# Optimization experiments

Measured on AMD Instinct MI355X. Metric: run time of the kernel, lower is better.

## Reference

```python
import jax, jax.numpy as jnp
import numpy as np

B, S, E = 4, 2048, 1024
H, HD, R = 16, 64, 32  # heads, head_dim, rank


def setup_inputs() -> dict:
    key = jax.random.key(0)
    ks = jax.random.split(key, 9)
    sc = 0.02
    return {
        "hidden_states": jax.random.normal(ks[0], (B, S, E), jnp.float32),
        "q_weight": jax.random.normal(ks[1], (E, E), jnp.float32) * sc,
        "q_bias": jax.random.normal(ks[2], (E,), jnp.float32) * sc,
        "k_weight": jax.random.normal(ks[3], (E, E), jnp.float32) * sc,
        "k_bias": jax.random.normal(ks[4], (E,), jnp.float32) * sc,
        "low_rank_value_weight": jax.random.normal(ks[5], (E, H * R), jnp.float32) * sc,
        "low_rank_value_bias": jax.random.normal(ks[6], (H * R,), jnp.float32) * sc,
        "low_rank_output_weight": jax.random.normal(ks[7], (H * R, E), jnp.float32) * sc,
        "output_bias": jax.random.normal(ks[8], (E,), jnp.float32) * sc,
    }


def reference(hidden_states, q_weight, q_bias, k_weight, k_bias,
              low_rank_value_weight, low_rank_value_bias,
              low_rank_output_weight, output_bias):
    b, s, _ = hidden_states.shape
    q = hidden_states @ q_weight + q_bias                       # [B,S,E]
    k = hidden_states @ k_weight + k_bias                       # [B,S,E]
    v = hidden_states @ low_rank_value_weight + low_rank_value_bias  # [B,S,H*R]
    q = q.reshape(b, s, H, HD).transpose(0, 2, 1, 3)            # [B,H,S,HD]
    k = k.reshape(b, s, H, HD).transpose(0, 2, 1, 3)
    v = v.reshape(b, s, H, R).transpose(0, 2, 1, 3)             # [B,H,S,R]
    scores = jnp.einsum('bhqd,bhkd->bhqk', q, k) / jnp.sqrt(jnp.float32(HD))
    causal = jnp.tril(jnp.ones((s, s), dtype=bool))
    scores = jnp.where(causal, scores, jnp.finfo(scores.dtype).min)
    probs = jax.nn.softmax(scores, axis=-1)                     # [B,H,S,S]
    attn = jnp.einsum('bhqk,bhkr->bhqr', probs, v)              # [B,H,S,R]
    attn = attn.transpose(0, 2, 1, 3).reshape(b, s, H * R)      # [B,S,H*R]
    out = attn @ low_rank_output_weight + output_bias           # [B,S,E]
    return out
```

## Files before the change

kernel.cpp:

```cpp
#include <hip/hip_runtime.h>

typedef _Float16 f16;
typedef __attribute__((ext_vector_type(4))) float f4;
typedef __attribute__((ext_vector_type(4))) _Float16 h4;
typedef __attribute__((ext_vector_type(8))) _Float16 h8;
typedef __attribute__((ext_vector_type(4))) float f32x4;
typedef __attribute__((ext_vector_type(4))) unsigned int u4;

extern "C" __device__ __attribute__((const)) float __ocml_native_exp2_f32(float);
#define EXP2F __ocml_native_exp2_f32
#define L2E 1.4426950408889634f

#define SWZ(row, colByte) \
  (((row) << 7) + ((colByte) ^ (((((row) ^ ((row) >> 3))) & 7) << 4)))

#define GL16(gp, lp)                                                  \
  __builtin_amdgcn_global_load_lds(                                   \
      (const __attribute__((address_space(1))) unsigned int*)(gp),    \
      (__attribute__((address_space(3))) unsigned int*)(lp), 16, 0, 0)

__global__ __launch_bounds__(256) void prep(
    const float* __restrict__ hs, f16* __restrict__ hsf,
    const float* __restrict__ qw, const float* __restrict__ kw,
    const float* __restrict__ vw, const float* __restrict__ ow,
    f16* __restrict__ wqkv, f16* __restrict__ owt) {
  const int t = threadIdx.x;
  if (blockIdx.x < 2048) {
    const int n4 = 8192 * 1024 / 4;
    for (int i = blockIdx.x * 256 + t; i < n4; i += 2048 * 256) {
      const f4 v = ((const f4*)hs)[i];
      h4 h;
      h.x = (f16)v.x; h.y = (f16)v.y; h.z = (f16)v.z; h.w = (f16)v.w;
      ((h4*)hsf)[i] = h;
    }
    return;
  }
  __shared__ float tile[32][33];
  int bid = blockIdx.x - 2048;
  const float* in;
  f16* out;
  int R, C, bx, by;
  if (bid < 1024) {
    in = qw; out = wqkv; R = 1024; C = 1024; bx = bid & 31; by = bid >> 5;
  } else if (bid < 2048) {
    bid -= 1024;
    in = kw; out = wqkv + (size_t)1024 * 1024; R = 1024; C = 1024;
    bx = bid & 31; by = bid >> 5;
  } else if (bid < 2560) {
    bid -= 2048;
    in = vw; out = wqkv + (size_t)2048 * 1024; R = 1024; C = 512;
    bx = bid & 15; by = bid >> 4;
  } else {
    bid -= 2560;
    in = ow; out = owt; R = 512; C = 1024; bx = bid & 31; by = bid >> 5;
  }
  const int tx = t & 31, ty = t >> 5;
  const int bc = bx * 32, br = by * 32;
#pragma unroll
  for (int i = 0; i < 4; ++i)
    tile[ty + i * 8][tx] = in[(size_t)(br + ty + i * 8) * C + bc + tx];
  __syncthreads();
#pragma unroll
  for (int i = 0; i < 4; ++i)
    out[(size_t)(bc + ty + i * 8) * R + br + tx] = (f16)tile[tx][ty + i * 8];
}

__global__ __launch_bounds__(256) void hgemm_qkv(
    const f16* __restrict__ A, const f16* __restrict__ Bt,
    const float* __restrict__ qb, const float* __restrict__ kb,
    const float* __restrict__ vb,
    f16* __restrict__ qf, f16* __restrict__ kf, f16* __restrict__ vf) {
  __shared__ f16 As[2 * 128 * 32];
  __shared__ f16 Bs[2 * 128 * 32];
  const int K = 1024;
  const int id = blockIdx.x;
  const int xcd = id & 7, loc = id >> 3;
  const int grp = loc >> 5, inn = loc & 31;
  const int bnT = grp * 4 + (inn >> 3);
  const int bm = (xcd * 8 + (inn & 7)) * 128;
  const int bn = bnT * 128;
  const int t = threadIdx.x;
  const int lane = t & 63, wave = t >> 6;
  const int wr = wave >> 1, wc = wave & 1;
  const int lrow = lane & 15, lk = lane >> 4;
  const int srow = lane >> 2;
  const int sblk = (lane & 3) ^ ((srow ^ (srow >> 2)) & 3);

  f32x4 acc[4][4];
#pragma unroll
  for (int i = 0; i < 4; ++i)
#pragma unroll
    for (int j = 0; j < 4; ++j) acc[i][j] = (f32x4)0.f;

  auto stage = [&](int buf, int ktile) {
#pragma unroll
    for (int i = 0; i < 2; ++i) {
      const int rr = (wave * 2 + i) * 16 + srow;
      GL16(A + (size_t)(bm + rr) * K + ktile * 32 + sblk * 8,
           (char*)As + buf * 8192 + (wave * 2 + i) * 1024);
      GL16(Bt + (size_t)(bn + rr) * K + ktile * 32 + sblk * 8,
           (char*)Bs + buf * 8192 + (wave * 2 + i) * 1024);
    }
  };

  stage(0, 0);
  for (int kt = 0; kt < 32; ++kt) {
    const int cur = kt & 1;
    stage(cur ^ 1, (kt + 1) & 31);
    asm volatile("s_waitcnt vmcnt(4)" ::: "memory");
    __builtin_amdgcn_s_barrier();
    __builtin_amdgcn_sched_barrier(0);
    h8 af[4], bf[4];
#pragma unroll
    for (int f = 0; f < 4; ++f) {
      const int ra = wr * 64 + f * 16 + lrow;
      af[f] = *(const h8*)((char*)As + cur * 8192 + ra * 64 +
                           ((lk ^ ((ra ^ (ra >> 2)) & 3)) << 4));
      const int rb = wc * 64 + f * 16 + lrow;
      bf[f] = *(const h8*)((char*)Bs + cur * 8192 + rb * 64 +
                           ((lk ^ ((rb ^ (rb >> 2)) & 3)) << 4));
    }
#pragma unroll
    for (int i2 = 0; i2 < 4; ++i2)
#pragma unroll
      for (int j = 0; j < 4; ++j)
        acc[i2][j] = __builtin_amdgcn_mfma_f32_16x16x32_f16(af[i2], bf[j], acc[i2][j], 0, 0, 0);
    asm volatile("s_waitcnt lgkmcnt(0)" ::: "memory");
    __builtin_amdgcn_sched_barrier(0);
    __builtin_amdgcn_s_barrier();
  }

  const float* bias;
  int nbase;
  if (bnT < 8) { bias = qb; nbase = 0; }
  else if (bnT < 16) { bias = kb; nbase = 1024; }
  else { bias = vb; nbase = 2048; }

#pragma unroll
  for (int fi = 0; fi < 4; ++fi) {
#pragma unroll
    for (int j = 0; j < 4; ++j) {
      const int grow = bm + wr * 64 + fi * 16 + lk * 4 + j;
      const int bb = grow >> 11, ss = grow & 2047;
#pragma unroll
      for (int fj = 0; fj < 4; ++fj) {
        const int gcol = bn + wc * 64 + fj * 16 + lrow;
        const int nl = gcol - nbase;
        const float g = acc[fi][fj][j] + bias[nl];
        if (bnT < 8) {
          qf[((size_t)(bb * 16 + (nl >> 6)) * 2048 + ss) * 64 + (nl & 63)] = (f16)g;
        } else if (bnT < 16) {
          kf[((size_t)(bb * 16 + (nl >> 6)) * 2048 + ss) * 64 + (nl & 63)] = (f16)g;
        } else {
          vf[((size_t)(bb * 16 + (nl >> 5)) * 2048 + ss) * 32 + (nl & 31)] = (f16)g;
        }
      }
    }
  }
}

__global__ __launch_bounds__(256) void transpose_v(
    const f16* __restrict__ vf, f16* __restrict__ vfT) {
  __shared__ f16 tl[32][36];
  const int bh = blockIdx.x >> 6;
  const int st = (blockIdx.x & 63) * 32;
  const int t = threadIdx.x;
  const int row = t >> 3, cq = t & 7;
  {
    const h4 v = *(const h4*)(vf + ((size_t)bh * 2048 + st + row) * 32 + cq * 4);
    *(h4*)&tl[row][cq * 4] = v;
  }
  __syncthreads();
  {
    h4 v;
#pragma unroll
    for (int e = 0; e < 4; ++e) v[e] = tl[cq * 4 + e][row];
    *(h4*)(vfT + ((size_t)bh * 32 + row) * 2048 + st + cq * 4) = v;
  }
}

__global__ __launch_bounds__(256) void hgemm_out(
    const f16* __restrict__ A, const f16* __restrict__ Bt,
    const float* __restrict__ bias, float* __restrict__ outp,
    const int N, const int K) {
  __shared__ f16 As[128 * 40];
  __shared__ f16 Bs[128 * 40];
  const int id = blockIdx.x;
  const int swz = (id & 7) * 64 + (id >> 3);
  const int bn = (swz & 7) * 128;
  const int bm = (swz >> 3) * 128;
  const int t = threadIdx.x;
  const int lane = t & 63, wave = t >> 6;
  const int wr = wave >> 1, wc = wave & 1;
  const int lrow = lane & 15, lk = lane >> 4;

  f32x4 acc[4][4];
#pragma unroll
  for (int i = 0; i < 4; ++i)
#pragma unroll
    for (int j = 0; j < 4; ++j) acc[i][j] = (f32x4)0.f;

  for (int kt = 0; kt < K; kt += 32) {
#pragma unroll
    for (int i = 0; i < 2; ++i) {
      const int ch = t + i * 256;
      const int row = ch >> 2, part = ch & 3;
      *(u4*)&As[row * 40 + part * 8] =
          *(const u4*)(A + (size_t)(bm + row) * K + kt + part * 8);
      *(u4*)&Bs[row * 40 + part * 8] =
          *(const u4*)(Bt + (size_t)(bn + row) * K + kt + part * 8);
    }
    __syncthreads();
    h8 af[4], bf[4];
#pragma unroll
    for (int f = 0; f < 4; ++f) {
      af[f] = *(const h8*)&As[(wr * 64 + f * 16 + lrow) * 40 + lk * 8];
      bf[f] = *(const h8*)&Bs[(wc * 64 + f * 16 + lrow) * 40 + lk * 8];
    }
#pragma unroll
    for (int i = 0; i < 4; ++i)
#pragma unroll
      for (int j = 0; j < 4; ++j)
        acc[i][j] = __builtin_amdgcn_mfma_f32_16x16x32_f16(af[i], bf[j], acc[i][j], 0, 0, 0);
    __syncthreads();
  }

#pragma unroll
  for (int fi = 0; fi < 4; ++fi) {
#pragma unroll
    for (int j = 0; j < 4; ++j) {
      const int grow = bm + wr * 64 + fi * 16 + lk * 4 + j;
#pragma unroll
      for (int fj = 0; fj < 4; ++fj) {
        const int gcol = bn + wc * 64 + fj * 16 + lrow;
        outp[(size_t)grow * N + gcol] = acc[fi][fj][j] + bias[gcol];
      }
    }
  }
}

__global__ __launch_bounds__(256) void attn_mfma(
    const f16* __restrict__ qf, const f16* __restrict__ kf,
    const f16* __restrict__ vfT, f16* __restrict__ attf) {
  __shared__ f16 Ks[2][64 * 64];
  __shared__ f16 VsT[2][32 * 64];
  __shared__ f16 Ps[4 * 32 * 64];
  const int id = blockIdx.x;
  const int bh = id & 63;
  const int p = id >> 6;
  const int t = threadIdx.x;
  const int lane = t & 63, w = t >> 6;
  const int l15 = lane & 15, g = lane >> 4;
  const size_t kvbase = (size_t)bh * 2048;
  char* Pw = (char*)&Ps[w * 32 * 64];
  const int srow = t >> 3, sch = t & 7;
  const int b = bh >> 4, h = bh & 15;

  h8 ones;
#pragma unroll
  for (int e = 0; e < 8; ++e) ones[e] = (f16)1.0f;

#pragma unroll
  for (int run = 0; run < 2; ++run) {
    const int qblk = run ? p : 15 - p;
    const int qbase = qblk * 128;

    h8 qreg[2][2];
#pragma unroll
    for (int fj = 0; fj < 2; ++fj) {
      const int q = qbase + fj * 64 + w * 16 + l15;
#pragma unroll
      for (int ks = 0; ks < 2; ++ks) {
        h8 raw = *(const h8*)(qf + (kvbase + q) * 64 + ks * 32 + g * 8);
#pragma unroll
        for (int e = 0; e < 8; ++e) raw[e] = raw[e] * (f16)0.125f;
        qreg[fj][ks] = raw;
      }
    }

    f32x4 accO[2][2];
    f32x4 accL[2];
#pragma unroll
    for (int i = 0; i < 2; ++i) {
      accL[i] = (f32x4)0.f;
#pragma unroll
      for (int j = 0; j < 2; ++j) accO[i][j] = (f32x4)0.f;
    }
    float m2[2] = {-1.0e30f, -1.0e30f};

    const int ntiles = qblk * 2 + 2;

    {
      const u4 k0 = *(const u4*)(kf + (kvbase + srow) * 64 + sch * 8);
      const u4 k1 = *(const u4*)(kf + (kvbase + 32 + srow) * 64 + sch * 8);
      const u4 v0 = *(const u4*)(vfT + ((size_t)bh * 32 + srow) * 2048 + sch * 8);
      *(u4*)((char*)&Ks[0][0] + SWZ(srow, sch * 16)) = k0;
      *(u4*)((char*)&Ks[0][0] + SWZ(srow + 32, sch * 16)) = k1;
      *(u4*)((char*)&VsT[0][0] + SWZ(srow, sch * 16)) = v0;
    }
    __syncthreads();

    u4 kr0, kr1, vr0;
    for (int kt = 0; kt < ntiles; ++kt) {
      const int cur = kt & 1;
      const int kbase = kt * 64;
      const bool more = (kt + 1 < ntiles);
      if (more) {
        const int kb2 = kbase + 64;
        kr0 = *(const u4*)(kf + (kvbase + kb2 + srow) * 64 + sch * 8);
        kr1 = *(const u4*)(kf + (kvbase + kb2 + 32 + srow) * 64 + sch * 8);
        vr0 = *(const u4*)(vfT + ((size_t)bh * 32 + srow) * 2048 + kb2 + sch * 8);
      }

      f32x4 accS[4][2];
#pragma unroll
      for (int i = 0; i < 4; ++i)
#pragma unroll
        for (int j = 0; j < 2; ++j) accS[i][j] = (f32x4)0.f;
#pragma unroll
      for (int ks = 0; ks < 2; ++ks) {
#pragma unroll
        for (int fim = 0; fim < 4; ++fim) {
          const h8 af = *(const h8*)((char*)&Ks[cur][0] +
                                     SWZ(fim * 16 + l15, ks * 64 + g * 16));
#pragma unroll
          for (int fj = 0; fj < 2; ++fj)
            accS[fim][fj] = __builtin_amdgcn_mfma_f32_16x16x32_f16(
                af, qreg[fj][ks], accS[fim][fj], 0, 0, 0);
        }
      }

#pragma unroll
      for (int fj = 0; fj < 2; ++fj) {
        const int qg = qbase + fj * 64 + w * 16 + l15;
        const bool need_mask = (kbase + 63 > qbase + fj * 64 + w * 16);
        float sc[4][4];
#pragma unroll
        for (int fim = 0; fim < 4; ++fim)
#pragma unroll
          for (int j = 0; j < 4; ++j) {
            float v = accS[fim][fj][j];
            if (need_mask) {
              const int key = kbase + fim * 16 + g * 4 + j;
              v = (key <= qg) ? v : -1.0e30f;
            }
            sc[fim][j] = v;
          }
        const float a0 = fmaxf(fmaxf(sc[0][0], sc[0][1]), sc[0][2]);
        const float a1 = fmaxf(fmaxf(sc[0][3], sc[1][0]), sc[1][1]);
        const float a2 = fmaxf(fmaxf(sc[1][2], sc[1][3]), sc[2][0]);
        const float a3 = fmaxf(fmaxf(sc[2][1], sc[2][2]), sc[2][3]);
        const float a4 = fmaxf(fmaxf(sc[3][0], sc[3][1]), sc[3][2]);
        float mc = fmaxf(fmaxf(fmaxf(a0, a1), a2),
                         fmaxf(fmaxf(a3, a4), sc[3][3]));
        mc = fmaxf(mc, __shfl_xor(mc, 16));
        mc = fmaxf(mc, __shfl_xor(mc, 32));
        if (!__all(mc <= m2[fj] + 1.5f)) {
          const float mnew = fmaxf(m2[fj], mc);
          const float corr = __expf(m2[fj] - mnew);
          m2[fj] = mnew;
#pragma unroll
          for (int j = 0; j < 4; ++j) {
            const float c = __shfl(corr, g * 4 + j);
            accO[fj][0][j] *= c;
            accO[fj][1][j] *= c;
            accL[fj][j] *= c;
          }
        }
        const float nml = -m2[fj] * L2E;
#pragma unroll
        for (int fim = 0; fim < 4; ++fim) {
          h4 hp;
#pragma unroll
          for (int j = 0; j < 4; ++j)
            hp[j] = (f16)EXP2F(fmaf(sc[fim][j], L2E, nml));
          *(h4*)(Pw + SWZ(fj * 16 + l15, fim * 32 + g * 8)) = hp;
        }
      }

#pragma unroll
      for (int ks = 0; ks < 2; ++ks) {
        const h8 pa0 = *(const h8*)(Pw + SWZ(l15, ks * 64 + g * 16));
        const h8 pa1 = *(const h8*)(Pw + SWZ(16 + l15, ks * 64 + g * 16));
#pragma unroll
        for (int fr = 0; fr < 2; ++fr) {
          const h8 vb = *(const h8*)((char*)&VsT[cur][0] +
                                     SWZ(fr * 16 + l15, ks * 64 + g * 16));
          accO[0][fr] = __builtin_amdgcn_mfma_f32_16x16x32_f16(pa0, vb, accO[0][fr], 0, 0, 0);
          accO[1][fr] = __builtin_amdgcn_mfma_f32_16x16x32_f16(pa1, vb, accO[1][fr], 0, 0, 0);
        }
        accL[0] = __builtin_amdgcn_mfma_f32_16x16x32_f16(pa0, ones, accL[0], 0, 0, 0);
        accL[1] = __builtin_amdgcn_mfma_f32_16x16x32_f16(pa1, ones, accL[1], 0, 0, 0);
      }

      if (more) {
        *(u4*)((char*)&Ks[cur ^ 1][0] + SWZ(srow, sch * 16)) = kr0;
        *(u4*)((char*)&Ks[cur ^ 1][0] + SWZ(srow + 32, sch * 16)) = kr1;
        *(u4*)((char*)&VsT[cur ^ 1][0] + SWZ(srow, sch * 16)) = vr0;
      }
      __syncthreads();
    }

#pragma unroll
    for (int fo = 0; fo < 2; ++fo) {
#pragma unroll
      for (int j = 0; j < 4; ++j) {
        const float iv = 1.f / accL[fo][j];
        const int q = qbase + fo * 64 + w * 16 + g * 4 + j;
#pragma unroll
        for (int fr = 0; fr < 2; ++fr) {
          const int r = fr * 16 + l15;
          attf[((size_t)b * 2048 + q) * 512 + h * 32 + r] = (f16)(accO[fo][fr][j] * iv);
        }
      }
    }
    __syncthreads();
  }
}

extern "C" void kernel_launch(void* const* d_in, const int* in_sizes, int n_in,
                              void* d_out, int out_size, void* d_ws, size_t ws_size,
                              hipStream_t stream) {
  const float* hs = (const float*)d_in[0];
  const float* qw = (const float*)d_in[1];
  const float* qb = (const float*)d_in[2];
  const float* kw = (const float*)d_in[3];
  const float* kb = (const float*)d_in[4];
  const float* vw = (const float*)d_in[5];
  const float* vb = (const float*)d_in[6];
  const float* ow = (const float*)d_in[7];
  const float* ob = (const float*)d_in[8];
  float* out = (float*)d_out;
  char* ws = (char*)d_ws;

  f16* qf = (f16*)(ws);
  f16* kf = (f16*)(ws + ((size_t)16 << 20));
  f16* vf = (f16*)(ws + ((size_t)32 << 20));
  f16* vfT = (f16*)(ws + ((size_t)72 << 20));
  f16* attf = (f16*)(ws + ((size_t)40 << 20));
  f16* wqkv = (f16*)(ws + ((size_t)48 << 20));
  f16* owt = (f16*)(ws + ((size_t)53 << 20));
  f16* hsf = (f16*)(ws + ((size_t)56 << 20));

  prep<<<dim3(5120), 256, 0, stream>>>(hs, hsf, qw, kw, vw, ow, wqkv, owt);
  hgemm_qkv<<<dim3(1280), 256, 0, stream>>>(hsf, wqkv, qb, kb, vb, qf, kf, vf);
  transpose_v<<<dim3(4096), 256, 0, stream>>>(vf, vfT);
  attn_mfma<<<dim3(512), 256, 0, stream>>>(qf, kf, vfT, attf);
  hgemm_out<<<dim3(512), 256, 0, stream>>>(attf, owt, ob, out, 1024, 512);
}
```

Before: 162.9 us.

## Widen attention blocks to 512 threads with 256-query tiles and per-wave causal skip

The attention kernel now uses 8 waves per block, and each block covers 256 queries instead of 128, so every K/V tile loaded into shared memory is reused by twice as many queries. The grid is halved to 256 blocks. Each wave tracks the last key tile its own query rows need and skips MFMA and softmax work on tiles past its causal limit, so waves early in the block idle while later waves finish. The risks are fewer blocks than compute units, worse load balance from the larger causal pairing granularity, and more register pressure under the 512-thread launch bound.

After: 173.1 us. 1.06x slower.

```diff
diff --git a/kernel.cpp b/kernel.cpp
--- a/kernel.cpp
+++ b/kernel.cpp
@@ -239,12 +239,12 @@
   }
 }
 
-__global__ __launch_bounds__(256) void attn_mfma(
+__global__ __launch_bounds__(512) void attn_mfma(
     const f16* __restrict__ qf, const f16* __restrict__ kf,
     const f16* __restrict__ vfT, f16* __restrict__ attf) {
   __shared__ f16 Ks[2][64 * 64];
   __shared__ f16 VsT[2][32 * 64];
-  __shared__ f16 Ps[4 * 32 * 64];
+  __shared__ f16 Ps[8 * 32 * 64];
   const int id = blockIdx.x;
   const int bh = id & 63;
   const int p = id >> 6;
@@ -252,7 +252,7 @@
   const int lane = t & 63, w = t >> 6;
   const int l15 = lane & 15, g = lane >> 4;
   const size_t kvbase = (size_t)bh * 2048;
-  char* Pw = (char*)&Ps[w * 32 * 64];
+  char* Pw = (char*)Ps + w * 4096;
   const int srow = t >> 3, sch = t & 7;
   const int b = bh >> 4, h = bh & 15;
 
@@ -260,15 +260,17 @@
 #pragma unroll
   for (int e = 0; e < 8; ++e) ones[e] = (f16)1.0f;
 
-#pragma unroll
   for (int run = 0; run < 2; ++run) {
-    const int qblk = run ? p : 15 - p;
-    const int qbase = qblk * 128;
+    const int qblk = run ? p : 7 - p;
+    const int qbase = qblk * 256;
+    const int ntiles = qblk * 4 + 4;
+    const int wl0 = (qbase + w * 16 + 15) >> 6;
+    const int wl1 = (qbase + 128 + w * 16 + 15) >> 6;
 
     h8 qreg[2][2];
 #pragma unroll
     for (int fj = 0; fj < 2; ++fj) {
-      const int q = qbase + fj * 64 + w * 16 + l15;
+      const int q = qbase + fj * 128 + w * 16 + l15;
 #pragma unroll
       for (int ks = 0; ks < 2; ++ks) {
         h8 raw = *(const h8*)(qf + (kvbase + q) * 64 + ks * 32 + g * 8);
@@ -288,115 +290,124 @@
     }
     float m2[2] = {-1.0e30f, -1.0e30f};
 
-    const int ntiles = qblk * 2 + 2;
-
     {
       const u4 k0 = *(const u4*)(kf + (kvbase + srow) * 64 + sch * 8);
-      const u4 k1 = *(const u4*)(kf + (kvbase + 32 + srow) * 64 + sch * 8);
-      const u4 v0 = *(const u4*)(vfT + ((size_t)bh * 32 + srow) * 2048 + sch * 8);
       *(u4*)((char*)&Ks[0][0] + SWZ(srow, sch * 16)) = k0;
-      *(u4*)((char*)&Ks[0][0] + SWZ(srow + 32, sch * 16)) = k1;
-      *(u4*)((char*)&VsT[0][0] + SWZ(srow, sch * 16)) = v0;
+      if (t < 256) {
+        const u4 v0 = *(const u4*)(vfT + ((size_t)bh * 32 + (t >> 3)) * 2048 + sch * 8);
+        *(u4*)((char*)&VsT[0][0] + SWZ(t >> 3, sch * 16)) = v0;
+      }
     }
     __syncthreads();
 
-    u4 kr0, kr1, vr0;
+    u4 kr, vr;
     for (int kt = 0; kt < ntiles; ++kt) {
       const int cur = kt & 1;
       const int kbase = kt * 64;
       const bool more = (kt + 1 < ntiles);
       if (more) {
         const int kb2 = kbase + 64;
-        kr0 = *(const u4*)(kf + (kvbase + kb2 + srow) * 64 + sch * 8);
-        kr1 = *(const u4*)(kf + (kvbase + kb2 + 32 + srow) * 64 + sch * 8);
-        vr0 = *(const u4*)(vfT + ((size_t)bh * 32 + srow) * 2048 + kb2 + sch * 8);
-      }
-
-      f32x4 accS[4][2];
-#pragma unroll
-      for (int i = 0; i < 4; ++i)
-#pragma unroll
-        for (int j = 0; j < 2; ++j) accS[i][j] = (f32x4)0.f;
-#pragma unroll
-      for (int ks = 0; ks < 2; ++ks) {
-#pragma unroll
-        for (int fim = 0; fim < 4; ++fim) {
-          const h8 af = *(const h8*)((char*)&Ks[cur][0] +
-                                     SWZ(fim * 16 + l15, ks * 64 + g * 16));
-#pragma unroll
-          for (int fj = 0; fj < 2; ++fj)
-            accS[fim][fj] = __builtin_amdgcn_mfma_f32_16x16x32_f16(
-                af, qreg[fj][ks], accS[fim][fj], 0, 0, 0);
-        }
-      }
-
-#pragma unroll
-      for (int fj = 0; fj < 2; ++fj) {
-        const int qg = qbase + fj * 64 + w * 16 + l15;
-        const bool need_mask = (kbase + 63 > qbase + fj * 64 + w * 16);
-        float sc[4][4];
-#pragma unroll
-        for (int fim = 0; fim < 4; ++fim)
-#pragma unroll
-          for (int j = 0; j < 4; ++j) {
-            float v = accS[fim][fj][j];
-            if (need_mask) {
-              const int key = kbase + fim * 16 + g * 4 + j;
-              v = (key <= qg) ? v : -1.0e30f;
-            }
-            sc[fim][j] = v;
-          }
-        const float a0 = fmaxf(fmaxf(sc[0][0], sc[0][1]), sc[0][2]);
-        const float a1 = fmaxf(fmaxf(sc[0][3], sc[1][0]), sc[1][1]);
-        const float a2 = fmaxf(fmaxf(sc[1][2], sc[1][3]), sc[2][0]);
-        const float a3 = fmaxf(fmaxf(sc[2][1], sc[2][2]), sc[2][3]);
-        const float a4 = fmaxf(fmaxf(sc[3][0], sc[3][1]), sc[3][2]);
-        float mc = fmaxf(fmaxf(fmaxf(a0, a1), a2),
-                         fmaxf(fmaxf(a3, a4), sc[3][3]));
-        mc = fmaxf(mc, __shfl_xor(mc, 16));
-        mc = fmaxf(mc, __shfl_xor(mc, 32));
-        if (!__all(mc <= m2[fj] + 1.5f)) {
-          const float mnew = fmaxf(m2[fj], mc);
-          const float corr = __expf(m2[fj] - mnew);
-          m2[fj] = mnew;
-#pragma unroll
-          for (int j = 0; j < 4; ++j) {
-            const float c = __shfl(corr, g * 4 + j);
-            accO[fj][0][j] *= c;
-            accO[fj][1][j] *= c;
-            accL[fj][j] *= c;
+        kr = *(const u4*)(kf + (kvbase + kb2 + srow) * 64 + sch * 8);
+        if (t < 256)
+          vr = *(const u4*)(vfT + ((size_t)bh * 32 + (t >> 3)) * 2048 + kb2 + sch * 8);
+      }
+
+      if (kt <= wl1) {
+        const bool do0 = (kt <= wl0);
+
+        f32x4 accS[4][2];
+#pragma unroll
+        for (int i = 0; i < 4; ++i)
+#pragma unroll
+          for (int j = 0; j < 2; ++j) accS[i][j] = (f32x4)0.f;
+#pragma unroll
+        for (int ks = 0; ks < 2; ++ks) {
+#pragma unroll
+          for (int fim = 0; fim < 4; ++fim) {
+            const h8 af = *(const h8*)((char*)&Ks[cur][0] +
+                                       SWZ(fim * 16 + l15, ks * 64 + g * 16));
+            if (do0)
+              accS[fim][0] = __builtin_amdgcn_mfma_f32_16x16x32_f16(
+                  af, qreg[0][ks], accS[fim][0], 0, 0, 0);
+            accS[fim][1] = __builtin_amdgcn_mfma_f32_16x16x32_f16(
+                af, qreg[1][ks], accS[fim][1], 0, 0, 0);
           }
         }
-        const float nml = -m2[fj] * L2E;
-#pragma unroll
-        for (int fim = 0; fim < 4; ++fim) {
-          h4 hp;
-#pragma unroll
-          for (int j = 0; j < 4; ++j)
-            hp[j] = (f16)EXP2F(fmaf(sc[fim][j], L2E, nml));
-          *(h4*)(Pw + SWZ(fj * 16 + l15, fim * 32 + g * 8)) = hp;
+
+#pragma unroll
+        for (int fj = 0; fj < 2; ++fj) {
+          if (fj == 0 && !do0) continue;
+          const int qg = qbase + fj * 128 + w * 16 + l15;
+          const bool need_mask = (kbase + 63 > qbase + fj * 128 + w * 16);
+          float sc[4][4];
+#pragma unroll
+          for (int fim = 0; fim < 4; ++fim)
+#pragma unroll
+            for (int j = 0; j < 4; ++j) {
+              float v = accS[fim][fj][j];
+              if (need_mask) {
+                const int key = kbase + fim * 16 + g * 4 + j;
+                v = (key <= qg) ? v : -1.0e30f;
+              }
+              sc[fim][j] = v;
+            }
+          const float a0 = fmaxf(fmaxf(sc[0][0], sc[0][1]), sc[0][2]);
+          const float a1 = fmaxf(fmaxf(sc[0][3], sc[1][0]), sc[1][1]);
+          const float a2 = fmaxf(fmaxf(sc[1][2], sc[1][3]), sc[2][0]);
+          const float a3 = fmaxf(fmaxf(sc[2][1], sc[2][2]), sc[2][3]);
+          const float a4 = fmaxf(fmaxf(sc[3][0], sc[3][1]), sc[3][2]);
+          float mc = fmaxf(fmaxf(fmaxf(a0, a1), a2),
+                           fmaxf(fmaxf(a3, a4), sc[3][3]));
+          mc = fmaxf(mc, __shfl_xor(mc, 16));
+          mc = fmaxf(mc, __shfl_xor(mc, 32));
+          if (!__all(mc <= m2[fj] + 1.5f)) {
+            const float mnew = fmaxf(m2[fj], mc);
+            const float corr = __expf(m2[fj] - mnew);
+            m2[fj] = mnew;
+#pragma unroll
+            for (int j = 0; j < 4; ++j) {
+              const float c = __shfl(corr, g * 4 + j);
+              accO[fj][0][j] *= c;
+              accO[fj][1][j] *= c;
+              accL[fj][j] *= c;
+            }
+          }
+          const float nml = -m2[fj] * L2E;
+#pragma unroll
+          for (int fim = 0; fim < 4; ++fim) {
+            h4 hp;
+#pragma unroll
+            for (int j = 0; j < 4; ++j)
+              hp[j] = (f16)EXP2F(fmaf(sc[fim][j], L2E, nml));
+            *(h4*)(Pw + SWZ(fj * 16 + l15, fim * 32 + g * 8)) = hp;
+          }
         }
-      }
-
-#pragma unroll
-      for (int ks = 0; ks < 2; ++ks) {
-        const h8 pa0 = *(const h8*)(Pw + SWZ(l15, ks * 64 + g * 16));
-        const h8 pa1 = *(const h8*)(Pw + SWZ(16 + l15, ks * 64 + g * 16));
-#pragma unroll
-        for (int fr = 0; fr < 2; ++fr) {
-          const h8 vb = *(const h8*)((char*)&VsT[cur][0] +
-                                     SWZ(fr * 16 + l15, ks * 64 + g * 16));
-          accO[0][fr] = __builtin_amdgcn_mfma_f32_16x16x32_f16(pa0, vb, accO[0][fr], 0, 0, 0);
-          accO[1][fr] = __builtin_amdgcn_mfma_f32_16x16x32_f16(pa1, vb, accO[1][fr], 0, 0, 0);
+
+#pragma unroll
+        for (int ks = 0; ks < 2; ++ks) {
+          const h8 pa1 = *(const h8*)(Pw + SWZ(16 + l15, ks * 64 + g * 16));
+#pragma unroll
+          for (int fr = 0; fr < 2; ++fr) {
+            const h8 vb = *(const h8*)((char*)&VsT[cur][0] +
+                                       SWZ(fr * 16 + l15, ks * 64 + g * 16));
+            if (do0) {
+              const h8 pa0 = *(const h8*)(Pw + SWZ(l15, ks * 64 + g * 16));
+              accO[0][fr] = __builtin_amdgcn_mfma_f32_16x16x32_f16(pa0, vb, accO[0][fr], 0, 0, 0);
+            }
+            accO[1][fr] = __builtin_amdgcn_mfma_f32_16x16x32_f16(pa1, vb, accO[1][fr], 0, 0, 0);
+          }
+          if (do0) {
+            const h8 pa0 = *(const h8*)(Pw + SWZ(l15, ks * 64 + g * 16));
+            accL[0] = __builtin_amdgcn_mfma_f32_16x16x32_f16(pa0, ones, accL[0], 0, 0, 0);
+          }
+          accL[1] = __builtin_amdgcn_mfma_f32_16x16x32_f16(pa1, ones, accL[1], 0, 0, 0);
         }
-        accL[0] = __builtin_amdgcn_mfma_f32_16x16x32_f16(pa0, ones, accL[0], 0, 0, 0);
-        accL[1] = __builtin_amdgcn_mfma_f32_16x16x32_f16(pa1, ones, accL[1], 0, 0, 0);
       }
 
       if (more) {
-        *(u4*)((char*)&Ks[cur ^ 1][0] + SWZ(srow, sch * 16)) = kr0;
-        *(u4*)((char*)&Ks[cur ^ 1][0] + SWZ(srow + 32, sch * 16)) = kr1;
-        *(u4*)((char*)&VsT[cur ^ 1][0] + SWZ(srow, sch * 16)) = vr0;
+        *(u4*)((char*)&Ks[cur ^ 1][0] + SWZ(srow, sch * 16)) = kr;
+        if (t < 256)
+          *(u4*)((char*)&VsT[cur ^ 1][0] + SWZ(t >> 3, sch * 16)) = vr;
       }
       __syncthreads();
     }
@@ -406,7 +417,7 @@
 #pragma unroll
       for (int j = 0; j < 4; ++j) {
         const float iv = 1.f / accL[fo][j];
-        const int q = qbase + fo * 64 + w * 16 + g * 4 + j;
+        const int q = qbase + fo * 128 + w * 16 + g * 4 + j;
 #pragma unroll
         for (int fr = 0; fr < 2; ++fr) {
           const int r = fr * 16 + l15;
@@ -445,6 +456,6 @@
   prep<<<dim3(5120), 256, 0, stream>>>(hs, hsf, qw, kw, vw, ow, wqkv, owt);
   hgemm_qkv<<<dim3(1280), 256, 0, stream>>>(hsf, wqkv, qb, kb, vb, qf, kf, vf);
   transpose_v<<<dim3(4096), 256, 0, stream>>>(vf, vfT);
-  attn_mfma<<<dim3(512), 256, 0, stream>>>(qf, kf, vfT, attf);
+  attn_mfma<<<dim3(256), 512, 0, stream>>>(qf, kf, vfT, attf);
   hgemm_out<<<dim3(512), 256, 0, stream>>>(attf, owt, ob, out, 1024, 512);
 }
```

## Halve attention query tile to 64 rows and double grid size

Applied to the files above, without the earlier changes.

The attention kernel now processes 64 queries per block (16 per wave) instead of 128. The grid doubles to 1024 blocks, each still pairing a short and a long causal block for balance. This raises parallelism and occupancy through fewer registers and a smaller P buffer in shared memory. In exchange, each K/V tile loaded into shared memory is reused by half as many queries. The change also adds s_setprio around the MFMA sections and stops unrolling the run loop.

Result: slower. 177.1 us (+8.7%).

```diff
diff --git a/kernel.cpp b/kernel.cpp
--- a/kernel.cpp
+++ b/kernel.cpp
@@ -244,7 +244,7 @@
     const f16* __restrict__ vfT, f16* __restrict__ attf) {
   __shared__ f16 Ks[2][64 * 64];
   __shared__ f16 VsT[2][32 * 64];
-  __shared__ f16 Ps[4 * 32 * 64];
+  __shared__ f16 Ps[4 * 16 * 64];
   const int id = blockIdx.x;
   const int bh = id & 63;
   const int p = id >> 6;
@@ -252,7 +252,7 @@
   const int lane = t & 63, w = t >> 6;
   const int l15 = lane & 15, g = lane >> 4;
   const size_t kvbase = (size_t)bh * 2048;
-  char* Pw = (char*)&Ps[w * 32 * 64];
+  char* Pw = (char*)Ps + w * 2048;
   const int srow = t >> 3, sch = t & 7;
   const int b = bh >> 4, h = bh & 15;
 
@@ -260,35 +260,27 @@
 #pragma unroll
   for (int e = 0; e < 8; ++e) ones[e] = (f16)1.0f;
 
-#pragma unroll
   for (int run = 0; run < 2; ++run) {
-    const int qblk = run ? p : 15 - p;
-    const int qbase = qblk * 128;
-
-    h8 qreg[2][2];
-#pragma unroll
-    for (int fj = 0; fj < 2; ++fj) {
-      const int q = qbase + fj * 64 + w * 16 + l15;
-#pragma unroll
-      for (int ks = 0; ks < 2; ++ks) {
-        h8 raw = *(const h8*)(qf + (kvbase + q) * 64 + ks * 32 + g * 8);
-#pragma unroll
-        for (int e = 0; e < 8; ++e) raw[e] = raw[e] * (f16)0.125f;
-        qreg[fj][ks] = raw;
-      }
-    }
-
-    f32x4 accO[2][2];
-    f32x4 accL[2];
-#pragma unroll
-    for (int i = 0; i < 2; ++i) {
-      accL[i] = (f32x4)0.f;
-#pragma unroll
-      for (int j = 0; j < 2; ++j) accO[i][j] = (f32x4)0.f;
-    }
-    float m2[2] = {-1.0e30f, -1.0e30f};
-
-    const int ntiles = qblk * 2 + 2;
+    const int qblk = run ? p : 31 - p;
+    const int qbase = qblk * 64;
+    const int ntiles = qblk + 1;
+    const int qg = qbase + w * 16 + l15;
+
+    h8 qreg[2];
+#pragma unroll
+    for (int ks = 0; ks < 2; ++ks) {
+      h8 raw = *(const h8*)(qf + (kvbase + qg) * 64 + ks * 32 + g * 8);
+#pragma unroll
+      for (int e = 0; e < 8; ++e) raw[e] = raw[e] * (f16)0.125f;
+      qreg[ks] = raw;
+    }
+
+    f32x4 accO[2];
+    f32x4 accL;
+    accL = (f32x4)0.f;
+#pragma unroll
+    for (int j = 0; j < 2; ++j) accO[j] = (f32x4)0.f;
+    float m2 = -1.0e30f;
 
     {
       const u4 k0 = *(const u4*)(kf + (kvbase + srow) * 64 + sch * 8);
@@ -300,7 +292,7 @@
     }
     __syncthreads();
 
-    u4 kr0, kr1, vr0;
+    u4 kr0, kr1, vr;
     for (int kt = 0; kt < ntiles; ++kt) {
       const int cur = kt & 1;
       const int kbase = kt * 64;
@@ -309,37 +301,33 @@
         const int kb2 = kbase + 64;
         kr0 = *(const u4*)(kf + (kvbase + kb2 + srow) * 64 + sch * 8);
         kr1 = *(const u4*)(kf + (kvbase + kb2 + 32 + srow) * 64 + sch * 8);
-        vr0 = *(const u4*)(vfT + ((size_t)bh * 32 + srow) * 2048 + kb2 + sch * 8);
-      }
-
-      f32x4 accS[4][2];
-#pragma unroll
-      for (int i = 0; i < 4; ++i)
-#pragma unroll
-        for (int j = 0; j < 2; ++j) accS[i][j] = (f32x4)0.f;
+        vr = *(const u4*)(vfT + ((size_t)bh * 32 + srow) * 2048 + kb2 + sch * 8);
+      }
+
+      f32x4 accS[4];
+#pragma unroll
+      for (int i = 0; i < 4; ++i) accS[i] = (f32x4)0.f;
+      __builtin_amdgcn_s_setprio(1);
 #pragma unroll
       for (int ks = 0; ks < 2; ++ks) {
 #pragma unroll
         for (int fim = 0; fim < 4; ++fim) {
           const h8 af = *(const h8*)((char*)&Ks[cur][0] +
                                      SWZ(fim * 16 + l15, ks * 64 + g * 16));
-#pragma unroll
-          for (int fj = 0; fj < 2; ++fj)
-            accS[fim][fj] = __builtin_amdgcn_mfma_f32_16x16x32_f16(
-                af, qreg[fj][ks], accS[fim][fj], 0, 0, 0);
+          accS[fim] = __builtin_amdgcn_mfma_f32_16x16x32_f16(
+              af, qreg[ks], accS[fim], 0, 0, 0);
         }
       }
-
-#pragma unroll
-      for (int fj = 0; fj < 2; ++fj) {
-        const int qg = qbase + fj * 64 + w * 16 + l15;
-        const bool need_mask = (kbase + 63 > qbase + fj * 64 + w * 16);
+      __builtin_amdgcn_s_setprio(0);
+
+      {
+        const bool need_mask = (kbase + 63 > qbase + w * 16);
         float sc[4][4];
 #pragma unroll
         for (int fim = 0; fim < 4; ++fim)
 #pragma unroll
           for (int j = 0; j < 4; ++j) {
-            float v = accS[fim][fj][j];
+            float v = accS[fim][j];
             if (need_mask) {
               const int key = kbase + fim * 16 + g * 4 + j;
               v = (key <= qg) ? v : -1.0e30f;
@@ -355,63 +343,59 @@
                          fmaxf(fmaxf(a3, a4), sc[3][3]));
         mc = fmaxf(mc, __shfl_xor(mc, 16));
         mc = fmaxf(mc, __shfl_xor(mc, 32));
-        if (!__all(mc <= m2[fj] + 1.5f)) {
-          const float mnew = fmaxf(m2[fj], mc);
-          const float corr = __expf(m2[fj] - mnew);
-          m2[fj] = mnew;
+        if (!__all(mc <= m2 + 1.5f)) {
+          const float mnew = fmaxf(m2, mc);
+          const float corr = __expf(m2 - mnew);
+          m2 = mnew;
 #pragma unroll
           for (int j = 0; j < 4; ++j) {
             const float c = __shfl(corr, g * 4 + j);
-            accO[fj][0][j] *= c;
-            accO[fj][1][j] *= c;
-            accL[fj][j] *= c;
+            accO[0][j] *= c;
+            accO[1][j] *= c;
+            accL[j] *= c;
           }
         }
-        const float nml = -m2[fj] * L2E;
+        const float nml = -m2 * L2E;
 #pragma unroll
         for (int fim = 0; fim < 4; ++fim) {
           h4 hp;
 #pragma unroll
           for (int j = 0; j < 4; ++j)
             hp[j] = (f16)EXP2F(fmaf(sc[fim][j], L2E, nml));
-          *(h4*)(Pw + SWZ(fj * 16 + l15, fim * 32 + g * 8)) = hp;
+          *(h4*)(Pw + SWZ(l15, fim * 32 + g * 8)) = hp;
         }
       }
 
+      __builtin_amdgcn_s_setprio(1);
 #pragma unroll
       for (int ks = 0; ks < 2; ++ks) {
-        const h8 pa0 = *(const h8*)(Pw + SWZ(l15, ks * 64 + g * 16));
-        const h8 pa1 = *(const h8*)(Pw + SWZ(16 + l15, ks * 64 + g * 16));
+        const h8 pa = *(const h8*)(Pw + SWZ(l15, ks * 64 + g * 16));
 #pragma unroll
         for (int fr = 0; fr < 2; ++fr) {
           const h8 vb = *(const h8*)((char*)&VsT[cur][0] +
                                      SWZ(fr * 16 + l15, ks * 64 + g * 16));
-          accO[0][fr] = __builtin_amdgcn_mfma_f32_16x16x32_f16(pa0, vb, accO[0][fr], 0, 0, 0);
-          accO[1][fr] = __builtin_amdgcn_mfma_f32_16x16x32_f16(pa1, vb, accO[1][fr], 0, 0, 0);
+          accO[fr] = __builtin_amdgcn_mfma_f32_16x16x32_f16(pa, vb, accO[fr], 0, 0, 0);
         }
-        accL[0] = __builtin_amdgcn_mfma_f32_16x16x32_f16(pa0, ones, accL[0], 0, 0, 0);
-        accL[1] = __builtin_amdgcn_mfma_f32_16x16x32_f16(pa1, ones, accL[1], 0, 0, 0);
-      }
+        accL = __builtin_amdgcn_mfma_f32_16x16x32_f16(pa, ones, accL, 0, 0, 0);
+      }
+      __builtin_amdgcn_s_setprio(0);
 
       if (more) {
         *(u4*)((char*)&Ks[cur ^ 1][0] + SWZ(srow, sch * 16)) = kr0;
         *(u4*)((char*)&Ks[cur ^ 1][0] + SWZ(srow + 32, sch * 16)) = kr1;
-        *(u4*)((char*)&VsT[cur ^ 1][0] + SWZ(srow, sch * 16)) = vr0;
+        *(u4*)((char*)&VsT[cur ^ 1][0] + SWZ(srow, sch * 16)) = vr;
       }
       __syncthreads();
     }
 
 #pragma unroll
-    for (int fo = 0; fo < 2; ++fo) {
-#pragma unroll
-      for (int j = 0; j < 4; ++j) {
-        const float iv = 1.f / accL[fo][j];
-        const int q = qbase + fo * 64 + w * 16 + g * 4 + j;
-#pragma unroll
-        for (int fr = 0; fr < 2; ++fr) {
-          const int r = fr * 16 + l15;
-          attf[((size_t)b * 2048 + q) * 512 + h * 32 + r] = (f16)(accO[fo][fr][j] * iv);
-        }
+    for (int j = 0; j < 4; ++j) {
+      const float iv = 1.f / accL[j];
+      const int q = qbase + w * 16 + g * 4 + j;
+#pragma unroll
+      for (int fr = 0; fr < 2; ++fr) {
+        const int r = fr * 16 + l15;
+        attf[((size_t)b * 2048 + q) * 512 + h * 32 + r] = (f16)(accO[fr][j] * iv);
       }
     }
     __syncthreads();
@@ -445,6 +429,6 @@
   prep<<<dim3(5120), 256, 0, stream>>>(hs, hsf, qw, kw, vw, ow, wqkv, owt);
   hgemm_qkv<<<dim3(1280), 256, 0, stream>>>(hsf, wqkv, qb, kb, vb, qf, kf, vf);
   transpose_v<<<dim3(4096), 256, 0, stream>>>(vf, vfT);
-  attn_mfma<<<dim3(512), 256, 0, stream>>>(qf, kf, vfT, attf);
+  attn_mfma<<<dim3(1024), 256, 0, stream>>>(qf, kf, vfT, attf);
   hgemm_out<<<dim3(512), 256, 0, stream>>>(attf, owt, ob, out, 1024, 512);
 }
```
